# Performance work log

Measured on AMD Instinct MI355X. Metric: run time of the kernel, lower is better.

Reference implementation:

```python
import jax, jax.numpy as jnp
import numpy as np

EPS = 1e-5

def _ln(x, g, b):
    mu = x.mean(-1, keepdims=True)
    var = ((x - mu) ** 2).mean(-1, keepdims=True)
    return (x - mu) * jax.lax.rsqrt(var + EPS) * g + b

def setup_inputs() -> dict:
    B, K, D, H, T = 64, 64, 128, 128, 4
    key = jax.random.key(0)
    ks = jax.random.split(key, 20)
    s = 0.02
    inp = {
        "slots": jax.random.normal(ks[0], (B, K, D), jnp.float32),
        "edge_probs": jax.random.uniform(ks[1], (B, K, K), jnp.float32),
        "edge_types": jax.random.uniform(ks[2], (B, K, K, T), jnp.float32),
        # f_self: LayerNorm(D) -> Linear(D,H) -> ReLU -> Linear(H,D)
        "ls_g": jnp.ones((D,), jnp.float32),
        "ls_b": jnp.zeros((D,), jnp.float32),
        "ws1": jax.random.normal(ks[3], (D, H), jnp.float32) * s,
        "bs1": jnp.zeros((H,), jnp.float32),
        "ws2": jax.random.normal(ks[4], (H, D), jnp.float32) * s,
        "bs2": jnp.zeros((D,), jnp.float32),
        # f_inter[tau]: Linear(2D,H) -> ReLU -> Linear(H,H) -> ReLU -> Linear(H,D), stacked over T
        "wi1": jax.random.normal(ks[5], (T, 2 * D, H), jnp.float32) * s,
        "bi1": jnp.zeros((T, H), jnp.float32),
        "wi2": jax.random.normal(ks[6], (T, H, H), jnp.float32) * s,
        "bi2": jnp.zeros((T, H), jnp.float32),
        "wi3": jax.random.normal(ks[7], (T, H, D), jnp.float32) * s,
        "bi3": jnp.zeros((T, D), jnp.float32),
        # update_mlp: LayerNorm(2D) -> Linear(2D,H) -> ReLU -> Linear(H,D)
        "lu_g": jnp.ones((2 * D,), jnp.float32),
        "lu_b": jnp.zeros((2 * D,), jnp.float32),
        "wu1": jax.random.normal(ks[8], (2 * D, H), jnp.float32) * s,
        "bu1": jnp.zeros((H,), jnp.float32),
        "wu2": jax.random.normal(ks[9], (H, D), jnp.float32) * s,
        "bu2": jnp.zeros((D,), jnp.float32),
    }
    return inp

NUM_MP = 2

def reference(slots, edge_probs, edge_types, ls_g, ls_b, ws1, bs1, ws2, bs2,
              wi1, bi1, wi2, bi2, wi3, bi3, lu_g, lu_b, wu1, bu1, wu2, bu2):
    B, K, D = slots.shape
    T = edge_types.shape[-1]
    h = slots
    for _ in range(NUM_MP):
        # f_self
        delta_self = jax.nn.relu(_ln(h, ls_g, ls_b) @ ws1 + bs1) @ ws2 + bs2
        # all-pairs features: cat[b,i,j] = [h[b,i] (sender), h[b,j] (receiver)]
        sender = jnp.broadcast_to(h[:, :, None, :], (B, K, K, D))
        receiver = jnp.broadcast_to(h[:, None, :, :], (B, K, K, D))
        pair = jnp.concatenate([sender, receiver], axis=-1)  # [B,K,K,2D]
        delta_inter = jnp.zeros_like(h)
        for tau in range(T):
            x = jax.nn.relu(pair @ wi1[tau] + bi1[tau])
            x = jax.nn.relu(x @ wi2[tau] + bi2[tau])
            eff = x @ wi3[tau] + bi3[tau]  # [B,K,K,D]
            w = edge_probs[..., None] * edge_types[..., tau, None]  # [B,K,K,1]
            delta_inter = delta_inter + (eff * w).sum(axis=1)  # sum over sender i
        combined = jnp.concatenate([h + delta_self, delta_inter], axis=-1)
        update = jax.nn.relu(_ln(combined, lu_g, lu_b) @ wu1 + bu1) @ wu2 + bu2
        h = h + update  # residual=True
    return h
```

## Files before the change

kernel.cpp:

```cpp
#include <hip/hip_runtime.h>
#include <hip/hip_fp16.h>

#define BATCH 64
#define KSLOT 64
#define DDIM  128
#define HDIM  128
#define TTYPE 4
#define NSLOT (BATCH*KSLOT)
#define EPSLN 1e-5f
#define YROW  544

typedef _Float16 v8h __attribute__((ext_vector_type(8)));
typedef _Float16 v4h __attribute__((ext_vector_type(4)));
typedef _Float16 v2h __attribute__((ext_vector_type(2)));
typedef float    v4f __attribute__((ext_vector_type(4)));

__device__ __forceinline__ float waveAllSum(float v) {
    #pragma unroll
    for (int m = 1; m < 64; m <<= 1) v += __shfl_xor(v, m, 64);
    return v;
}

__global__ __launch_bounds__(256) void k_wconv(
        const float* __restrict__ ws1, const float* __restrict__ wi1,
        const float* __restrict__ ws2, const float* __restrict__ wu1,
        const float* __restrict__ wu2, const float* __restrict__ wi3,
        const float* __restrict__ wi2, const float* __restrict__ bi1,
        const float* __restrict__ bi3,
        const float* __restrict__ ep, const float* __restrict__ et,
        __half* __restrict__ ws1T, __half* __restrict__ wi1catT,
        __half* __restrict__ ws2T, __half* __restrict__ wu1T,
        __half* __restrict__ wu2T, __half* __restrict__ w3catT,
        __half* __restrict__ w2T16, float* __restrict__ biascat,
        __half* __restrict__ wPre) {
    __shared__ __align__(16) float tile[128*132];
    int bx = blockIdx.x, tid = threadIdx.x;
    if (bx >= 22) {
        int bx2 = bx - 22, b = bx2 >> 2, chunk = bx2 & 3;
        const float4* etb = (const float4*)(et + (size_t)b*16384);
        const float*  epb = ep + (size_t)b*4096;
        __half* w0 = wPre + ((size_t)0*BATCH + b)*4096;
        __half* w1 = wPre + ((size_t)1*BATCH + b)*4096;
        __half* w2 = wPre + ((size_t)2*BATCH + b)*4096;
        __half* w3 = wPre + ((size_t)3*BATCH + b)*4096;
        int c0 = chunk*1024;
        for (int c = c0 + tid; c < c0 + 1024; c += 256) {
            float wv = epb[c];
            float4 e = etb[c];
            w0[c] = __float2half(wv * e.x);
            w1[c] = __float2half(wv * e.y);
            w2[c] = __float2half(wv * e.z);
            w3[c] = __float2half(wv * e.w);
        }
        return;
    }
    if (bx == 21) {
        for (int idx = tid; idx < 128*32; idx += 256) {
            int o = idx >> 5, c = idx & 31;
            w3catT[(size_t)o*YROW + 512 + c] = (c < 4) ? __float2half(bi3[c*DDIM + o]) : __float2half(0.f);
        }
        for (int idx = tid; idx < 1024; idx += 256) {
            int th = idx >> 7, o = idx & 127;
            biascat[idx] = (th & 1) ? bi1[(th>>1)*HDIM + o] : 0.f;
        }
        return;
    }
    const float* src; __half* dst; int dstride = 128, dcol = 0;
    if (bx == 0)      { src = ws1; dst = ws1T; }
    else if (bx <= 8) { int th = bx-1, tau = th>>1, half = th&1;
                        src = wi1 + ((size_t)tau*256 + half*128)*128;
                        dst = wi1catT + (size_t)th*128*128; }
    else if (bx == 9) { src = ws2; dst = ws2T; }
    else if (bx ==10) { src = wu2; dst = wu2T; }
    else if (bx <=12) { int hh = bx-11; src = wu1 + (size_t)hh*128*128;
                        dst = wu1T; dstride = 256; dcol = hh*128; }
    else if (bx <=16) { int tau = bx-13; src = wi3 + (size_t)tau*16384;
                        dst = w3catT; dstride = YROW; dcol = tau*128; }
    else              { int tau = bx-17; src = wi2 + (size_t)tau*16384;
                        dst = w2T16 + (size_t)tau*16384; }
    for (int idx = tid; idx < 4096; idx += 256) {
        int r = idx >> 5, c4 = idx & 31;
        *(float4*)&tile[r*132 + c4*4] = *(const float4*)&src[(size_t)r*128 + c4*4];
    }
    __syncthreads();
    for (int idx = tid; idx < 8192; idx += 256) {
        int n = idx >> 6, kp = idx & 63;
        __half2 p = __floats2half2_rn(tile[(2*kp)*132 + n], tile[(2*kp+1)*132 + n]);
        *(__half2*)&dst[(size_t)n*dstride + dcol + 2*kp] = p;
    }
}

#define LROW 136
__global__ __launch_bounds__(512, 4) void k_pair(
        const float* __restrict__ h,
        const __half* __restrict__ wi1catT,
        const float* __restrict__ biascat,
        const __half* __restrict__ w2T16,
        const float* __restrict__ bi2,
        const __half* __restrict__ wPre,
        __half* __restrict__ Ycat) {
    __shared__ __align__(16) _Float16 U[HDIM*LROW];
    __shared__ __align__(16) _Float16 Cs[KSLOT*LROW];
    __shared__ __align__(16) _Float16 As[KSLOT*LROW];
    __shared__ __align__(16) _Float16 wS[KSLOT*KSLOT];
    int bx = blockIdx.x, b = bx >> 2, tau = bx & 3;
    int tid = threadIdx.x, lane = tid & 63, w = tid >> 6;
    int jt = w >> 1, oh = w & 1, quad = lane >> 4, n = lane & 15;

    {
        int row = tid >> 3, c0 = (tid & 7)*16;
        const float* hp = &h[(size_t)(b*KSLOT + row)*128 + c0];
        #pragma unroll
        for (int q = 0; q < 4; q++) {
            float4 f = *(const float4*)&hp[q*4];
            *(__half2*)&U[row*LROW + c0 + q*4]     = __floats2half2_rn(f.x, f.y);
            *(__half2*)&U[row*LROW + c0 + q*4 + 2] = __floats2half2_rn(f.z, f.w);
        }
    }
    {
        int base = tid*8;
        *(v8h*)&wS[base] = *(const v8h*)&wPre[((size_t)tau*BATCH + b)*4096 + base];
    }
    __syncthreads();

    {
        int hf = w >> 2, rt = w & 3;
        const __half* wb = wi1catT + (size_t)(tau*2 + hf)*128*128;
        const float* bcp = biascat + (tau*2 + hf)*128;
        _Float16* dst = hf ? Cs : As;
        v8h afr[4];
        #pragma unroll
        for (int ks = 0; ks < 4; ks++)
            afr[ks] = *(const v8h*)&U[(rt*16 + n)*LROW + ks*32 + quad*8];
        #pragma unroll
        for (int ot = 0; ot < 8; ot++) {
            float b0 = bcp[ot*16 + n];
            v4f acc = (v4f){b0, b0, b0, b0};
            #pragma unroll
            for (int ks = 0; ks < 4; ks++)
                acc = __builtin_amdgcn_mfma_f32_16x16x32_f16(
                    afr[ks], *(const v8h*)&wb[(size_t)(ot*16 + n)*128 + ks*32 + quad*8], acc, 0, 0, 0);
            #pragma unroll
            for (int r = 0; r < 4; r++)
                dst[(rt*16 + quad*4 + r)*LROW + ot*16 + n] = (_Float16)acc[r];
        }
    }
    __syncthreads();
    #pragma unroll
    for (int k2 = 0; k2 < 4; k2++) {
        int idx = tid + k2*512;
        int o = idx >> 4, seg = (idx & 15)*8;
        *(v8h*)&U[o*LROW + seg] = *(const v8h*)&w2T16[((size_t)tau*128 + o)*128 + seg];
    }
    __syncthreads();

    v8h cfrag[4];
    #pragma unroll
    for (int ks = 0; ks < 4; ks++)
        cfrag[ks] = *(const v8h*)&Cs[(jt*16 + n)*LROW + ks*32 + quad*8];
    v4f biasvec[4];
    #pragma unroll
    for (int ot = 0; ot < 4; ot++) {
        float b0 = bi2[tau*HDIM + oh*64 + ot*16 + n];
        biasvec[ot] = (v4f){b0, b0, b0, b0};
    }

    v4h yacch[4];
    #pragma unroll
    for (int ot = 0; ot < 4; ot++) yacch[ot] = (v4h){0,0,0,0};
    v4h wsacch = (v4h){0,0,0,0};
    const v8h zero8 = {0,0,0,0,0,0,0,0};
    const v4h zero4h = {0,0,0,0};

    const _Float16* ub = &U[(oh*64 + n)*LROW + quad*8];

    for (int i = 0; i < KSLOT; ++i) {
        v8h a[4];
        #pragma unroll
        for (int ks = 0; ks < 4; ks++)
            a[ks] = *(const v8h*)&As[i*LROW + ks*32 + quad*8];
        v4h wv = *(const v4h*)&wS[i*KSLOT + jt*16 + quad*4];
        v8h x1[4];
        #pragma unroll
        for (int ks = 0; ks < 4; ks++)
            x1[ks] = __builtin_elementwise_max(a[ks] + cfrag[ks], zero8);
        v4f acc0 = biasvec[0], acc1 = biasvec[1], acc2 = biasvec[2], acc3 = biasvec[3];
        #pragma unroll
        for (int ks = 0; ks < 4; ks++) {
            acc0 = __builtin_amdgcn_mfma_f32_16x16x32_f16(x1[ks], *(const v8h*)(ub + 0*16*LROW + ks*32), acc0, 0, 0, 0);
            acc1 = __builtin_amdgcn_mfma_f32_16x16x32_f16(x1[ks], *(const v8h*)(ub + 1*16*LROW + ks*32), acc1, 0, 0, 0);
            acc2 = __builtin_amdgcn_mfma_f32_16x16x32_f16(x1[ks], *(const v8h*)(ub + 2*16*LROW + ks*32), acc2, 0, 0, 0);
            acc3 = __builtin_amdgcn_mfma_f32_16x16x32_f16(x1[ks], *(const v8h*)(ub + 3*16*LROW + ks*32), acc3, 0, 0, 0);
        }
        #define EPI(ACC, OT) { \
            v2h lo = __builtin_bit_cast(v2h, __builtin_amdgcn_cvt_pkrtz(ACC[0], ACC[1])); \
            v2h hi = __builtin_bit_cast(v2h, __builtin_amdgcn_cvt_pkrtz(ACC[2], ACC[3])); \
            v4h rel = {lo[0], lo[1], hi[0], hi[1]}; \
            rel = __builtin_elementwise_max(rel, zero4h); \
            yacch[OT] = yacch[OT] + wv * rel; }
        EPI(acc0, 0) EPI(acc1, 1) EPI(acc2, 2) EPI(acc3, 3)
        #undef EPI
        wsacch = wsacch + wv;
    }

    #pragma unroll
    for (int r = 0; r < 4; r++) {
        int j = jt*16 + quad*4 + r;
        __half* yb = Ycat + (size_t)(b*KSLOT + j)*YROW + tau*128 + oh*64;
        #pragma unroll
        for (int ot = 0; ot < 4; ot++)
            yb[ot*16 + n] = __float2half((float)yacch[ot][r]);
    }
    if (oh == 0 && n == 0) {
        #pragma unroll
        for (int r = 0; r < 4; r++)
            Ycat[(size_t)(b*KSLOT + jt*16 + quad*4 + r)*YROW + 512 + tau] = __float2half((float)wsacch[r]);
    }
    if (tau == 0 && oh == 1 && n == 0) {
        const v4h z4 = {0,0,0,0};
        #pragma unroll
        for (int r = 0; r < 4; r++) {
            _Float16* pz = (_Float16*)(Ycat + (size_t)(b*KSLOT + jt*16 + quad*4 + r)*YROW + 516);
            #pragma unroll
            for (int c = 0; c < 28; c += 4) *(v4h*)&pz[c] = z4;
        }
    }
}

__global__ __launch_bounds__(512, 2) void k_mega(
        const __half* __restrict__ Ycat, const __half* __restrict__ w3catT,
        const float* __restrict__ ls_g, const float* __restrict__ ls_b,
        const __half* __restrict__ ws1T, const float* __restrict__ bs1,
        const __half* __restrict__ ws2T, const float* __restrict__ bs2,
        const float* __restrict__ g, const float* __restrict__ bb,
        const __half* __restrict__ wu1T, const float* __restrict__ bu1,
        const __half* __restrict__ wu2T, const float* __restrict__ bu2,
        const float* __restrict__ h, float* __restrict__ hout) {
    __shared__ __align__(16) _Float16 Ys[16*552];
    __shared__ __align__(16) float    Crow[16*260];
    __shared__ __align__(16) float    Hrow[16*132];
    __shared__ __align__(16) _Float16 Xs[16*136];
    __shared__ __align__(16) _Float16 Ts[16*136];
    __shared__ __align__(16) _Float16 Xa[16*264];
    __shared__ __align__(16) _Float16 Ut[16*136];
    int tid = threadIdx.x, lane = tid & 63, w = tid >> 6;
    int n = lane & 15, quad = lane >> 4;
    int row0 = blockIdx.x*16;

    for (int u = tid; u < 1024; u += 512) {
        int r = u >> 6, seg = (u & 63)*8;
        *(v8h*)&Ys[r*552 + seg] = *(const v8h*)&Ycat[(size_t)(row0 + r)*YROW + seg];
    }
    if (tid < 64) {
        int r = tid >> 2, seg = 512 + (tid & 3)*8;
        *(v8h*)&Ys[r*552 + seg] = *(const v8h*)&Ycat[(size_t)(row0 + r)*YROW + seg];
    }
    {
        int r = tid >> 5, c4 = (tid & 31)*4;
        *(float4*)&Hrow[r*132 + c4] = *(const float4*)&h[(size_t)(row0 + r)*128 + c4];
    }
    __syncthreads();
    {
        const __half* wp = w3catT + (size_t)(w*16 + n)*YROW + quad*8;
        const _Float16* yp = &Ys[n*552 + quad*8];
        v4f acc = (v4f){0.f,0.f,0.f,0.f};
        #pragma unroll 4
        for (int ks = 0; ks < 17; ks++) {
            v8h a  = *(const v8h*)(yp + ks*32);
            v8h bf = *(const v8h*)(wp + ks*32);
            acc = __builtin_amdgcn_mfma_f32_16x16x32_f16(a, bf, acc, 0, 0, 0);
        }
        #pragma unroll
        for (int r = 0; r < 4; r++)
            Crow[(quad*4 + r)*260 + 128 + w*16 + n] = acc[r];
    }
    #pragma unroll
    for (int rr = 0; rr < 2; rr++) {
        int r = w*2 + rr;
        float x0 = Hrow[r*132 + 2*lane], x1 = Hrow[r*132 + 2*lane + 1];
        float mu = waveAllSum(x0 + x1) * (1.f/128.f);
        float d0 = x0 - mu, d1 = x1 - mu;
        float var = waveAllSum(d0*d0 + d1*d1) * (1.f/128.f);
        float rs = rsqrtf(var + EPSLN);
        float2 gv = *(const float2*)&ls_g[2*lane];
        float2 bv = *(const float2*)&ls_b[2*lane];
        *(__half2*)&Xs[r*136 + 2*lane] = __floats2half2_rn(d0*rs*gv.x + bv.x, d1*rs*gv.y + bv.y);
    }
    __syncthreads();
    {
        float b0 = bs1[w*16 + n];
        v4f acc = (v4f){b0, b0, b0, b0};
        const __half* wp = ws1T + (size_t)(w*16 + n)*128 + quad*8;
        #pragma unroll
        for (int ks = 0; ks < 4; ks++) {
            v8h a  = *(const v8h*)&Xs[n*136 + ks*32 + quad*8];
            v8h bf = *(const v8h*)(wp + ks*32);
            acc = __builtin_amdgcn_mfma_f32_16x16x32_f16(a, bf, acc, 0, 0, 0);
        }
        #pragma unroll
        for (int r = 0; r < 4; r++)
            Ts[(quad*4 + r)*136 + w*16 + n] = (_Float16)fmaxf(acc[r], 0.f);
    }
    __syncthreads();
    {
        float b0 = bs2[w*16 + n];
        v4f acc = (v4f){b0, b0, b0, b0};
        const __half* wp = ws2T + (size_t)(w*16 + n)*128 + quad*8;
        #pragma unroll
        for (int ks = 0; ks < 4; ks++) {
            v8h a  = *(const v8h*)&Ts[n*136 + ks*32 + quad*8];
            v8h bf = *(const v8h*)(wp + ks*32);
            acc = __builtin_amdgcn_mfma_f32_16x16x32_f16(a, bf, acc, 0, 0, 0);
        }
        #pragma unroll
        for (int r = 0; r < 4; r++) {
            int rr = quad*4 + r, col = w*16 + n;
            Crow[rr*260 + col] = Hrow[rr*132 + col] + acc[r];
        }
    }
    __syncthreads();
    #pragma unroll
    for (int rr = 0; rr < 2; rr++) {
        int r = w*2 + rr;
        float4 v = *(const float4*)&Crow[r*260 + 4*lane];
        float mu = waveAllSum(v.x + v.y + v.z + v.w) * (1.f/256.f);
        float d0 = v.x-mu, d1 = v.y-mu, d2 = v.z-mu, d3 = v.w-mu;
        float var = waveAllSum(d0*d0 + d1*d1 + d2*d2 + d3*d3) * (1.f/256.f);
        float rs = rsqrtf(var + EPSLN);
        float4 gv = *(const float4*)&g[4*lane];
        float4 bv = *(const float4*)&bb[4*lane];
        *(__half2*)&Xa[r*264 + 4*lane]     = __floats2half2_rn(d0*rs*gv.x + bv.x, d1*rs*gv.y + bv.y);
        *(__half2*)&Xa[r*264 + 4*lane + 2] = __floats2half2_rn(d2*rs*gv.z + bv.z, d3*rs*gv.w + bv.w);
    }
    __syncthreads();
    {
        float b0 = bu1[w*16 + n];
        v4f acc = (v4f){b0, b0, b0, b0};
        const __half* wp = wu1T + (size_t)(w*16 + n)*256 + quad*8;
        const _Float16* xp = &Xa[n*264 + quad*8];
        #pragma unroll 4
        for (int ks = 0; ks < 8; ks++) {
            v8h a  = *(const v8h*)(xp + ks*32);
            v8h bf = *(const v8h*)(wp + ks*32);
            acc = __builtin_amdgcn_mfma_f32_16x16x32_f16(a, bf, acc, 0, 0, 0);
        }
        #pragma unroll
        for (int r = 0; r < 4; r++)
            Ut[(quad*4 + r)*136 + w*16 + n] = (_Float16)fmaxf(acc[r], 0.f);
    }
    __syncthreads();
    {
        float b0 = bu2[w*16 + n];
        v4f acc = (v4f){b0, b0, b0, b0};
        const __half* wp = wu2T + (size_t)(w*16 + n)*128 + quad*8;
        #pragma unroll
        for (int ks = 0; ks < 4; ks++) {
            v8h a  = *(const v8h*)&Ut[n*136 + ks*32 + quad*8];
            v8h bf = *(const v8h*)(wp + ks*32);
            acc = __builtin_amdgcn_mfma_f32_16x16x32_f16(a, bf, acc, 0, 0, 0);
        }
        #pragma unroll
        for (int r = 0; r < 4; r++) {
            int rr = quad*4 + r, col = w*16 + n;
            hout[(size_t)(row0 + rr)*128 + col] = Hrow[rr*132 + col] + acc[r];
        }
    }
}

extern "C" void kernel_launch(void* const* d_in, const int* in_sizes, int n_in,
                              void* d_out, int out_size, void* d_ws, size_t ws_size,
                              hipStream_t stream) {
    const float* slots = (const float*)d_in[0];
    const float* ep    = (const float*)d_in[1];
    const float* et    = (const float*)d_in[2];
    const float* ls_g  = (const float*)d_in[3];
    const float* ls_b  = (const float*)d_in[4];
    const float* ws1   = (const float*)d_in[5];
    const float* bs1   = (const float*)d_in[6];
    const float* ws2   = (const float*)d_in[7];
    const float* bs2   = (const float*)d_in[8];
    const float* wi1   = (const float*)d_in[9];
    const float* bi1   = (const float*)d_in[10];
    const float* wi2   = (const float*)d_in[11];
    const float* bi2   = (const float*)d_in[12];
    const float* wi3   = (const float*)d_in[13];
    const float* bi3   = (const float*)d_in[14];
    const float* lu_g  = (const float*)d_in[15];
    const float* lu_b  = (const float*)d_in[16];
    const float* wu1   = (const float*)d_in[17];
    const float* bu1   = (const float*)d_in[18];
    const float* wu2   = (const float*)d_in[19];
    const float* bu2   = (const float*)d_in[20];
    float* out = (float*)d_out;

    char* p = (char*)d_ws;
    float*  h_buf   = (float*)p;   p += (size_t)NSLOT*DDIM*4;
    __half* Ycat    = (__half*)p;  p += (size_t)NSLOT*YROW*2;
    __half* wPre    = (__half*)p;  p += (size_t)TTYPE*BATCH*4096*2;
    __half* ws1T    = (__half*)p;  p += 128*128*2;
    __half* wi1catT = (__half*)p;  p += 1024*128*2;
    __half* ws2T    = (__half*)p;  p += 128*128*2;
    __half* wu1T    = (__half*)p;  p += 128*256*2;
    __half* wu2T    = (__half*)p;  p += 128*128*2;
    __half* w3catT  = (__half*)p;  p += 128*YROW*2;
    __half* w2T16   = (__half*)p;  p += 4*128*128*2;
    float*  biascat = (float*)p;   p += 1024*4;

    k_wconv<<<22 + 256, 256, 0, stream>>>(ws1, wi1, ws2, wu1, wu2, wi3, wi2, bi1, bi3,
                                          ep, et, ws1T, wi1catT, ws2T, wu1T, wu2T,
                                          w3catT, w2T16, biascat, wPre);

    for (int mp = 0; mp < 2; mp++) {
        const float* h = (mp == 0) ? slots : h_buf;
        float* hout = (mp == 0) ? h_buf : out;
        k_pair<<<BATCH*TTYPE, 512, 0, stream>>>(h, wi1catT, biascat, w2T16, bi2, wPre, Ycat);
        k_mega<<<NSLOT/16, 512, 0, stream>>>(Ycat, w3catT, ls_g, ls_b, ws1T, bs1, ws2T, bs2,
                                             lu_g, lu_b, wu1T, bu1, wu2T, bu2, h, hout);
    }
}
```

Measured before the change: 223.0 us.

## Split k_pair over receiver halves and sender halves with LDS reduction

```diff
diff --git a/kernel.cpp b/kernel.cpp
--- a/kernel.cpp
+++ b/kernel.cpp
@@ -100,12 +100,14 @@
         const __half* __restrict__ wPre,
         __half* __restrict__ Ycat) {
     __shared__ __align__(16) _Float16 U[HDIM*LROW];
-    __shared__ __align__(16) _Float16 Cs[KSLOT*LROW];
+    __shared__ __align__(16) _Float16 Cs[32*LROW];
     __shared__ __align__(16) _Float16 As[KSLOT*LROW];
-    __shared__ __align__(16) _Float16 wS[KSLOT*KSLOT];
-    int bx = blockIdx.x, b = bx >> 2, tau = bx & 3;
+    __shared__ __align__(16) _Float16 wS[KSLOT*32];
+    int bx = blockIdx.x;
+    int jhalf = bx & 1, tau = (bx >> 1) & 3, b = bx >> 3;
     int tid = threadIdx.x, lane = tid & 63, w = tid >> 6;
-    int jt = w >> 1, oh = w & 1, quad = lane >> 4, n = lane & 15;
+    int quad = lane >> 4, n = lane & 15;
+    int ihalf = w & 1, oh = (w >> 1) & 1, jt = w >> 2;
 
     {
         int row = tid >> 3, c0 = (tid & 7)*16;
@@ -117,21 +119,24 @@
             *(__half2*)&U[row*LROW + c0 + q*4 + 2] = __floats2half2_rn(f.z, f.w);
         }
     }
-    {
-        int base = tid*8;
-        *(v8h*)&wS[base] = *(const v8h*)&wPre[((size_t)tau*BATCH + b)*4096 + base];
-    }
-    __syncthreads();
-
-    {
-        int hf = w >> 2, rt = w & 3;
-        const __half* wb = wi1catT + (size_t)(tau*2 + hf)*128*128;
-        const float* bcp = biascat + (tau*2 + hf)*128;
-        _Float16* dst = hf ? Cs : As;
+    if (tid < 256) {
+        int i = tid >> 2, seg = (tid & 3)*8;
+        *(v8h*)&wS[i*32 + seg] =
+            *(const v8h*)&wPre[((size_t)tau*BATCH + b)*4096 + i*64 + jhalf*32 + seg];
+    }
+    __syncthreads();
+
+    if (w < 6) {
+        int isA = (w < 4);
+        int rt  = isA ? w : (w - 4);
+        int hrow0 = isA ? rt*16 : (jhalf*32 + rt*16);
+        const __half* wb = wi1catT + (size_t)(tau*2 + (isA ? 0 : 1))*128*128;
+        const float* bcp = biascat + (tau*2 + (isA ? 0 : 1))*128;
+        _Float16* dst = isA ? (As + rt*16*LROW) : (Cs + rt*16*LROW);
         v8h afr[4];
         #pragma unroll
         for (int ks = 0; ks < 4; ks++)
-            afr[ks] = *(const v8h*)&U[(rt*16 + n)*LROW + ks*32 + quad*8];
+            afr[ks] = *(const v8h*)&U[(hrow0 + n)*LROW + ks*32 + quad*8];
         #pragma unroll
         for (int ot = 0; ot < 8; ot++) {
             float b0 = bcp[ot*16 + n];
@@ -142,7 +147,7 @@
                     afr[ks], *(const v8h*)&wb[(size_t)(ot*16 + n)*128 + ks*32 + quad*8], acc, 0, 0, 0);
             #pragma unroll
             for (int r = 0; r < 4; r++)
-                dst[(rt*16 + quad*4 + r)*LROW + ot*16 + n] = (_Float16)acc[r];
+                dst[(quad*4 + r)*LROW + ot*16 + n] = (_Float16)acc[r];
         }
     }
     __syncthreads();
@@ -173,13 +178,15 @@
     const v4h zero4h = {0,0,0,0};
 
     const _Float16* ub = &U[(oh*64 + n)*LROW + quad*8];
-
-    for (int i = 0; i < KSLOT; ++i) {
+    int ibase = ihalf*32;
+
+    for (int ii = 0; ii < 32; ++ii) {
+        int i = ibase + ii;
         v8h a[4];
         #pragma unroll
         for (int ks = 0; ks < 4; ks++)
             a[ks] = *(const v8h*)&As[i*LROW + ks*32 + quad*8];
-        v4h wv = *(const v4h*)&wS[i*KSLOT + jt*16 + quad*4];
+        v4h wv = *(const v4h*)&wS[i*32 + jt*16 + quad*4];
         v8h x1[4];
         #pragma unroll
         for (int ks = 0; ks < 4; ks++)
@@ -203,26 +210,44 @@
         wsacch = wsacch + wv;
     }
 
-    #pragma unroll
-    for (int r = 0; r < 4; r++) {
-        int j = jt*16 + quad*4 + r;
-        __half* yb = Ycat + (size_t)(b*KSLOT + j)*YROW + tau*128 + oh*64;
-        #pragma unroll
-        for (int ot = 0; ot < 4; ot++)
-            yb[ot*16 + n] = __float2half((float)yacch[ot][r]);
-    }
-    if (oh == 0 && n == 0) {
-        #pragma unroll
-        for (int r = 0; r < 4; r++)
-            Ycat[(size_t)(b*KSLOT + jt*16 + quad*4 + r)*YROW + 512 + tau] = __float2half((float)wsacch[r]);
-    }
-    if (tau == 0 && oh == 1 && n == 0) {
-        const v4h z4 = {0,0,0,0};
+    __syncthreads();
+    v4h* sc = (v4h*)As;
+    int scbase = ((jt*2 + oh)*64 + lane)*5;
+    if (ihalf == 1) {
+        #pragma unroll
+        for (int ot = 0; ot < 4; ot++) sc[scbase + ot] = yacch[ot];
+        sc[scbase + 4] = wsacch;
+    }
+    __syncthreads();
+    if (ihalf == 0) {
+        #pragma unroll
+        for (int ot = 0; ot < 4; ot++) yacch[ot] = yacch[ot] + sc[scbase + ot];
+        wsacch = wsacch + sc[scbase + 4];
+
         #pragma unroll
         for (int r = 0; r < 4; r++) {
-            _Float16* pz = (_Float16*)(Ycat + (size_t)(b*KSLOT + jt*16 + quad*4 + r)*YROW + 516);
+            int j = jhalf*32 + jt*16 + quad*4 + r;
+            __half* yb = Ycat + (size_t)(b*KSLOT + j)*YROW + tau*128 + oh*64;
             #pragma unroll
-            for (int c = 0; c < 28; c += 4) *(v4h*)&pz[c] = z4;
+            for (int ot = 0; ot < 4; ot++)
+                yb[ot*16 + n] = __float2half((float)yacch[ot][r]);
+        }
+        if (oh == 0 && n == 0) {
+            #pragma unroll
+            for (int r = 0; r < 4; r++) {
+                int j = jhalf*32 + jt*16 + quad*4 + r;
+                Ycat[(size_t)(b*KSLOT + j)*YROW + 512 + tau] = __float2half((float)wsacch[r]);
+            }
+        }
+        if (tau == 0 && oh == 1 && n == 0) {
+            const v4h z4 = {0,0,0,0};
+            #pragma unroll
+            for (int r = 0; r < 4; r++) {
+                int j = jhalf*32 + jt*16 + quad*4 + r;
+                _Float16* pz = (_Float16*)(Ycat + (size_t)(b*KSLOT + j)*YROW + 516);
+                #pragma unroll
+                for (int c = 0; c < 28; c += 4) *(v4h*)&pz[c] = z4;
+            }
         }
     }
 }
@@ -413,7 +438,7 @@
     for (int mp = 0; mp < 2; mp++) {
         const float* h = (mp == 0) ? slots : h_buf;
         float* hout = (mp == 0) ? h_buf : out;
-        k_pair<<<BATCH*TTYPE, 512, 0, stream>>>(h, wi1catT, biascat, w2T16, bi2, wPre, Ycat);
+        k_pair<<<BATCH*TTYPE*2, 512, 0, stream>>>(h, wi1catT, biascat, w2T16, bi2, wPre, Ycat);
         k_mega<<<NSLOT/16, 512, 0, stream>>>(Ycat, w3catT, ls_g, ls_b, ws1T, bs1, ws2T, bs2,
                                              lu_g, lu_b, wu1T, bu1, wu2T, bu2, h, hout);
     }
```

Result: faster. 217.0 us (-2.7%).
